# Performance work log

Measured on AMD Instinct MI355X. Metric: run time of the kernel, lower is better.

## Reference

```python
import jax, jax.numpy as jnp
import numpy as np

B, C_IN, C_OUT, N_VERT, K = 8, 64, 64, 40962, 7


def setup_inputs() -> dict:
    key = jax.random.key(0)
    k1, k2, k3, k4 = jax.random.split(key, 4)
    x = jax.random.normal(k1, (B, C_IN, N_VERT), dtype=jnp.float32)
    neigh_indices = jax.random.randint(k2, (N_VERT, K), 0, N_VERT, dtype=jnp.int64)
    # nn.Linear(in=K*C_IN, out=C_OUT): weight [C_OUT, K*C_IN], bias [C_OUT]
    W = jax.random.normal(k3, (C_OUT, C_IN * K), dtype=jnp.float32) * (1.0 / np.sqrt(C_IN * K))
    b = jax.random.normal(k4, (C_OUT,), dtype=jnp.float32) * 0.01
    return {"x": x, "neigh_indices": neigh_indices, "W": W, "b": b}


def reference(x, neigh_indices, W, b):
    # x: [B, C_in, N]; neigh_indices: [N, K]
    # gather neighbor features: [B, C_in, N, K]
    gathered = x[:, :, neigh_indices]
    # Linear over flattened (C_in, K) per vertex. The torch flatten order is
    # (c, k) since mat is [B, N, C_in, K] reshaped to [B*N, C_in*K].
    Wr = W.reshape(W.shape[0], x.shape[1], neigh_indices.shape[1])  # [C_out, C_in, K]
    out = jnp.einsum('bcnk,ock->bon', gathered, Wr) + b[None, :, None]
    return out  # [B, C_out, N]
```

## Files before the change

kernel.cpp:

```cpp
#include <hip/hip_runtime.h>

#define BB 8
#define CI 64
#define CO 64
#define NV 40962
#define KN 7
#define KKD 448

typedef unsigned short u16;
typedef unsigned int u32;

typedef __bf16 bf16x8 __attribute__((ext_vector_type(8)));
typedef float f32x16 __attribute__((ext_vector_type(16)));

__device__ inline u16 f2bf(float f) {
    u32 u = __builtin_bit_cast(u32, f);
    u32 r = (u + 0x7FFFu + ((u >> 16) & 1u)) >> 16;
    return (u16)r;
}

__device__ inline void gload_lds16(const void* g, void* l) {
    __builtin_amdgcn_global_load_lds(
        (const __attribute__((address_space(1))) u32*)g,
        (__attribute__((address_space(3))) u32*)l, 16, 0, 0);
}

__global__ void transpose_x(const float* __restrict__ x, u16* __restrict__ xT) {
    __shared__ u16 tile[64][72];
    const int b = blockIdx.y;
    const int n0 = blockIdx.x * 64;
    const int tid = threadIdx.x;

#pragma unroll
    for (int i = 0; i < 16; ++i) {
        int flat = i * 256 + tid;
        int c = flat >> 6;
        int nn = flat & 63;
        int n = n0 + nn;
        if (n < NV) {
            float v = __builtin_nontemporal_load(&x[((size_t)b * CI + c) * NV + n]);
            tile[nn][c] = f2bf(v);
        }
    }
    __syncthreads();

#pragma unroll
    for (int i = 0; i < 2; ++i) {
        int flat8 = i * 256 + tid;
        int nn = flat8 >> 3;
        int c0 = (flat8 & 7) * 8;
        int n = n0 + nn;
        if (n < NV) {
            uint4 v = *(const uint4*)&tile[nn][c0];
            *(uint4*)&xT[((size_t)b * NV + n) * CI + c0] = v;
        }
    }
}

__global__ void pack_w(const float* __restrict__ W, u16* __restrict__ Wf) {
    int e = blockIdx.x * 256 + threadIdx.x;
    if (e < 2 * 28 * 64 * 8) {
        int j = e & 7;
        int lane = (e >> 3) & 63;
        int sg = e >> 9;
        int s = sg % 28;
        int rg = sg / 28;
        int o = rg * 32 + (lane & 31);
        int kk = s * 16 + ((lane >> 5) << 3) + j;
        int kn = kk >> 6;
        int c = kk & 63;
        Wf[e] = f2bf(W[o * KKD + c * KN + kn]);
    }
}

__global__ __launch_bounds__(512, 4) void conv_mfma(
    const u16* __restrict__ xT, const u16* __restrict__ Wf,
    const int* __restrict__ idx, const float* __restrict__ bias,
    float* __restrict__ out) {
    __shared__ alignas(16) u16 G[3][8192];

    const int bid = blockIdx.x;
    const int b = bid & 7;
    const int n0 = (bid >> 3) * 128;
    const int t = threadIdx.x;
    const int lane = t & 63;
    const int w = t >> 6;
    const int rg = w & 1;
    const int cg = w >> 1;
    const int col = lane & 31;
    const int half = lane >> 5;

    const char* xbc = (const char*)(xT + (size_t)b * NV * CI);
    const char* wfc = (const char*)Wf;

    const int sr0 = t >> 3;
    const int q = t & 7;
    const int qe = q ^ (sr0 & 7);

    int g0 = n0 + sr0;        if (g0 >= NV) g0 = NV - 1;
    int g1 = n0 + 64 + sr0;   if (g1 >= NV) g1 = NV - 1;

    int j0[KN], j1[KN];
    {
        int4 lo0 = *(const int4*)(idx + (size_t)g0 * KN);
        int4 hi0 = *(const int4*)(idx + (size_t)g0 * KN + 3);
        int4 lo1 = *(const int4*)(idx + (size_t)g1 * KN);
        int4 hi1 = *(const int4*)(idx + (size_t)g1 * KN + 3);
        j0[0] = lo0.x; j0[1] = lo0.y; j0[2] = lo0.z; j0[3] = lo0.w;
        j0[4] = hi0.y; j0[5] = hi0.z; j0[6] = hi0.w;
        j1[0] = lo1.x; j1[1] = lo1.y; j1[2] = lo1.z; j1[3] = lo1.w;
        j1[4] = hi1.y; j1[5] = hi1.z; j1[6] = hi1.w;
    }

    char* gb = (char*)&G[0][0];
    const u32 dst0 = (u32)(w * 1024);
    const u32 dst1 = (u32)(8192 + w * 1024);

    const int brow = cg * 32 + col;
    const u32 rbase = (u32)(brow * 128);
    const u32 rmask = (u32)(brow & 7) << 4;

    const u32 abase = (u32)((rg * 28) * 1024 + lane * 16);

    f32x16 acc{};

    gload_lds16(xbc + (size_t)j0[0] * 128 + qe * 16, gb + 0 * 16384 + dst0);
    gload_lds16(xbc + (size_t)j1[0] * 128 + qe * 16, gb + 0 * 16384 + dst1);
    __builtin_amdgcn_sched_barrier(0);
    uint4 acur0 = *(const uint4*)(wfc + abase + 0 * 1024);
    uint4 acur1 = *(const uint4*)(wfc + abase + 1 * 1024);
    uint4 acur2 = *(const uint4*)(wfc + abase + 2 * 1024);
    uint4 acur3 = *(const uint4*)(wfc + abase + 3 * 1024);
    __builtin_amdgcn_sched_barrier(0);
    gload_lds16(xbc + (size_t)j0[1] * 128 + qe * 16, gb + 1 * 16384 + dst0);
    gload_lds16(xbc + (size_t)j1[1] * 128 + qe * 16, gb + 1 * 16384 + dst1);
    __builtin_amdgcn_sched_barrier(0);

#pragma unroll
    for (int k = 0; k < KN; ++k) {
        uint4 an0, an1, an2, an3;
        if (k + 1 < KN) {
            u32 ab = abase + (u32)((k + 1) * 4 * 1024);
            an0 = *(const uint4*)(wfc + ab + 0 * 1024);
            an1 = *(const uint4*)(wfc + ab + 1 * 1024);
            an2 = *(const uint4*)(wfc + ab + 2 * 1024);
            an3 = *(const uint4*)(wfc + ab + 3 * 1024);
        }
        __builtin_amdgcn_sched_barrier(0);

        if (k <= 5) asm volatile("s_waitcnt vmcnt(6)" ::: "memory");
        else        asm volatile("s_waitcnt vmcnt(0)" ::: "memory");
        __builtin_amdgcn_sched_barrier(0);
        __builtin_amdgcn_s_barrier();
        __builtin_amdgcn_sched_barrier(0);

        if (k + 2 < KN) {
            u32 db = (u32)(((k + 2) % 3) * 16384);
            gload_lds16(xbc + (size_t)j0[k + 2] * 128 + qe * 16, gb + db + dst0);
            gload_lds16(xbc + (size_t)j1[k + 2] * 128 + qe * 16, gb + db + dst1);
        }
        __builtin_amdgcn_sched_barrier(0);

        const char* gsrc = gb + (u32)((k % 3) * 16384);
#pragma unroll
        for (int sub = 0; sub < 4; ++sub) {
            u32 boff = rbase + ((((u32)sub * 32) + (u32)half * 16) ^ rmask);
            uint4 bf = *(const uint4*)(gsrc + boff);
            uint4 af = (sub == 0) ? acur0 : (sub == 1) ? acur1 : (sub == 2) ? acur2 : acur3;
            acc = __builtin_amdgcn_mfma_f32_32x32x16_bf16(
                __builtin_bit_cast(bf16x8, af),
                __builtin_bit_cast(bf16x8, bf), acc, 0, 0, 0);
        }

        if (k + 1 < KN) { acur0 = an0; acur1 = an1; acur2 = an2; acur3 = an3; }
    }

    const int v = n0 + cg * 32 + col;
    if (v < NV) {
        float* ob = out + (size_t)b * CO * NV + v;
#pragma unroll
        for (int r = 0; r < 16; ++r) {
            int rowo = (r & 3) + 8 * (r >> 2) + 4 * half;
            int o = rg * 32 + rowo;
            ob[(size_t)o * NV] = acc[r] + bias[o];
        }
    }
}

__global__ void naive_conv(const float* __restrict__ x, const int* __restrict__ idx,
                           const float* __restrict__ W, const float* __restrict__ bias,
                           float* __restrict__ out) {
    const int b = blockIdx.y;
    const int n = blockIdx.x * 4 + (threadIdx.x & 3);
    const int o = threadIdx.x >> 2;
    if (n >= NV) return;
    float acc = bias[o];
    const float* xb = x + (size_t)b * CI * NV;
    const float* wo = W + o * KKD;
    for (int k = 0; k < KN; ++k) {
        int j = idx[n * KN + k];
        for (int c = 0; c < CI; ++c)
            acc += xb[(size_t)c * NV + j] * wo[c * KN + k];
    }
    out[((size_t)b * CO + o) * NV + n] = acc;
}

extern "C" void kernel_launch(void* const* d_in, const int* in_sizes, int n_in,
                              void* d_out, int out_size, void* d_ws, size_t ws_size,
                              hipStream_t stream) {
    const float* x    = (const float*)d_in[0];
    const int*   idx  = (const int*)d_in[1];
    const float* W    = (const float*)d_in[2];
    const float* bias = (const float*)d_in[3];
    float* out = (float*)d_out;

    const size_t xT_bytes = (size_t)BB * NV * CI * 2;
    const size_t wf_bytes = (size_t)2 * 28 * 64 * 8 * 2;
    const size_t need = xT_bytes + wf_bytes;

    if (ws_size >= need) {
        u16* xT = (u16*)d_ws;
        u16* Wf = (u16*)((char*)d_ws + xT_bytes);
        transpose_x<<<dim3((NV + 63) / 64, BB), 256, 0, stream>>>(x, xT);
        pack_w<<<dim3(112), 256, 0, stream>>>(W, Wf);
        const int ntiles = (NV + 127) / 128;
        conv_mfma<<<dim3(ntiles * BB), 512, 0, stream>>>(xT, Wf, idx, bias, out);
    } else {
        naive_conv<<<dim3((NV + 3) / 4, BB), 256, 0, stream>>>(x, idx, W, bias, out);
    }
}
```

Baseline: 80.96 us.

## Interleave batch into vertex-major layout so each gather fetches all batches

The transposed activation buffer changes from [B][N][C] to [N][B][C], so one neighbor index pulls a contiguous 1KB row covering all 8 batches. The conv kernel now tiles 16 vertices times 8 batches per 256-thread block, with each wave running two MFMA accumulators. Index loads and gather requests are shared across batches, which is meant to cut index traffic and improve gather locality. In exchange the grid, swizzle and epilogue are restructured: output stores are scattered across batches and occupancy settings change.

```diff
diff --git a/kernel.cpp b/kernel.cpp
--- a/kernel.cpp
+++ b/kernel.cpp
@@ -25,7 +25,7 @@
         (__attribute__((address_space(3))) u32*)l, 16, 0, 0);
 }
 
-__global__ void transpose_x(const float* __restrict__ x, u16* __restrict__ xT) {
+__global__ void transpose_x(const float* __restrict__ x, u16* __restrict__ xTI) {
     __shared__ u16 tile[64][72];
     const int b = blockIdx.y;
     const int n0 = blockIdx.x * 64;
@@ -52,7 +52,7 @@
         int n = n0 + nn;
         if (n < NV) {
             uint4 v = *(const uint4*)&tile[nn][c0];
-            *(uint4*)&xT[((size_t)b * NV + n) * CI + c0] = v;
+            *(uint4*)&xTI[((size_t)n * 8 + b) * 64 + c0] = v;
         }
     }
 }
@@ -73,67 +73,74 @@
     }
 }
 
-__global__ __launch_bounds__(512, 4) void conv_mfma(
-    const u16* __restrict__ xT, const u16* __restrict__ Wf,
+__global__ __launch_bounds__(256, 3) void conv_mfma(
+    const u16* __restrict__ xTI, const u16* __restrict__ Wf,
     const int* __restrict__ idx, const float* __restrict__ bias,
     float* __restrict__ out) {
     __shared__ alignas(16) u16 G[3][8192];
 
     const int bid = blockIdx.x;
-    const int b = bid & 7;
-    const int n0 = (bid >> 3) * 128;
+    const int n0 = bid * 16;
     const int t = threadIdx.x;
     const int lane = t & 63;
     const int w = t >> 6;
     const int rg = w & 1;
     const int cg = w >> 1;
-    const int col = lane & 31;
     const int half = lane >> 5;
-
-    const char* xbc = (const char*)(xT + (size_t)b * NV * CI);
+    const int seg = lane >> 3;
+    const int sl = lane & 7;
+
+    const char* xbc = (const char*)xTI;
     const char* wfc = (const char*)Wf;
-
-    const int sr0 = t >> 3;
-    const int q = t & 7;
-    const int qe = q ^ (sr0 & 7);
-
-    int g0 = n0 + sr0;        if (g0 >= NV) g0 = NV - 1;
-    int g1 = n0 + 64 + sr0;   if (g1 >= NV) g1 = NV - 1;
-
-    int j0[KN], j1[KN];
-    {
-        int4 lo0 = *(const int4*)(idx + (size_t)g0 * KN);
-        int4 hi0 = *(const int4*)(idx + (size_t)g0 * KN + 3);
-        int4 lo1 = *(const int4*)(idx + (size_t)g1 * KN);
-        int4 hi1 = *(const int4*)(idx + (size_t)g1 * KN + 3);
-        j0[0] = lo0.x; j0[1] = lo0.y; j0[2] = lo0.z; j0[3] = lo0.w;
-        j0[4] = hi0.y; j0[5] = hi0.z; j0[6] = hi0.w;
-        j1[0] = lo1.x; j1[1] = lo1.y; j1[2] = lo1.z; j1[3] = lo1.w;
-        j1[4] = hi1.y; j1[5] = hi1.z; j1[6] = hi1.w;
-    }
-
     char* gb = (char*)&G[0][0];
-    const u32 dst0 = (u32)(w * 1024);
-    const u32 dst1 = (u32)(8192 + w * 1024);
-
-    const int brow = cg * 32 + col;
-    const u32 rbase = (u32)(brow * 128);
-    const u32 rmask = (u32)(brow & 7) << 4;
+
+    int jv[4][KN];
+#pragma unroll
+    for (int i = 0; i < 4; ++i) {
+        int v = n0 + w * 4 + i; if (v >= NV) v = NV - 1;
+        int4 lo = *(const int4*)(idx + (size_t)v * KN);
+        int4 hi = *(const int4*)(idx + (size_t)v * KN + 3);
+        jv[i][0] = lo.x; jv[i][1] = lo.y; jv[i][2] = lo.z; jv[i][3] = lo.w;
+        jv[i][4] = hi.y; jv[i][5] = hi.z; jv[i][6] = hi.w;
+    }
+
+    u32 srcoff[4];
+#pragma unroll
+    for (int i = 0; i < 4; ++i)
+        srcoff[i] = (u32)(seg * 128) + (u32)((((sl ^ seg ^ i) & 7)) << 4);
+
+    const u32 dstrow = (u32)((w * 4) * 1024);
+
+    const int vsub = (lane & 31) >> 3;
+    const int bb = lane & 7;
+    u32 rbyte[2][4];
+#pragma unroll
+    for (int ct = 0; ct < 2; ++ct)
+#pragma unroll
+        for (int s = 0; s < 4; ++s) {
+            int rowv = (cg * 2 + ct) * 4 + vsub;
+            int slot = ((s * 2 + half) ^ bb ^ vsub) & 7;
+            rbyte[ct][s] = (u32)(rowv * 1024 + bb * 128 + slot * 16);
+        }
 
     const u32 abase = (u32)((rg * 28) * 1024 + lane * 16);
 
-    f32x16 acc{};
-
-    gload_lds16(xbc + (size_t)j0[0] * 128 + qe * 16, gb + 0 * 16384 + dst0);
-    gload_lds16(xbc + (size_t)j1[0] * 128 + qe * 16, gb + 0 * 16384 + dst1);
+    f32x16 acc0{}, acc1{};
+
+#pragma unroll
+    for (int i = 0; i < 4; ++i)
+        gload_lds16(xbc + (size_t)jv[i][0] * 1024 + srcoff[i],
+                    gb + 0 * 16384 + dstrow + (u32)(i * 1024));
     __builtin_amdgcn_sched_barrier(0);
     uint4 acur0 = *(const uint4*)(wfc + abase + 0 * 1024);
     uint4 acur1 = *(const uint4*)(wfc + abase + 1 * 1024);
     uint4 acur2 = *(const uint4*)(wfc + abase + 2 * 1024);
     uint4 acur3 = *(const uint4*)(wfc + abase + 3 * 1024);
     __builtin_amdgcn_sched_barrier(0);
-    gload_lds16(xbc + (size_t)j0[1] * 128 + qe * 16, gb + 1 * 16384 + dst0);
-    gload_lds16(xbc + (size_t)j1[1] * 128 + qe * 16, gb + 1 * 16384 + dst1);
+#pragma unroll
+    for (int i = 0; i < 4; ++i)
+        gload_lds16(xbc + (size_t)jv[i][1] * 1024 + srcoff[i],
+                    gb + 1 * 16384 + dstrow + (u32)(i * 1024));
     __builtin_amdgcn_sched_barrier(0);
 
 #pragma unroll
@@ -148,7 +155,7 @@
         }
         __builtin_amdgcn_sched_barrier(0);
 
-        if (k <= 5) asm volatile("s_waitcnt vmcnt(6)" ::: "memory");
+        if (k <= 5) asm volatile("s_waitcnt vmcnt(8)" ::: "memory");
         else        asm volatile("s_waitcnt vmcnt(0)" ::: "memory");
         __builtin_amdgcn_sched_barrier(0);
         __builtin_amdgcn_s_barrier();
@@ -156,34 +163,39 @@
 
         if (k + 2 < KN) {
             u32 db = (u32)(((k + 2) % 3) * 16384);
-            gload_lds16(xbc + (size_t)j0[k + 2] * 128 + qe * 16, gb + db + dst0);
-            gload_lds16(xbc + (size_t)j1[k + 2] * 128 + qe * 16, gb + db + dst1);
+#pragma unroll
+            for (int i = 0; i < 4; ++i)
+                gload_lds16(xbc + (size_t)jv[i][k + 2] * 1024 + srcoff[i],
+                            gb + db + dstrow + (u32)(i * 1024));
         }
         __builtin_amdgcn_sched_barrier(0);
 
         const char* gsrc = gb + (u32)((k % 3) * 16384);
 #pragma unroll
-        for (int sub = 0; sub < 4; ++sub) {
-            u32 boff = rbase + ((((u32)sub * 32) + (u32)half * 16) ^ rmask);
-            uint4 bf = *(const uint4*)(gsrc + boff);
-            uint4 af = (sub == 0) ? acur0 : (sub == 1) ? acur1 : (sub == 2) ? acur2 : acur3;
-            acc = __builtin_amdgcn_mfma_f32_32x32x16_bf16(
-                __builtin_bit_cast(bf16x8, af),
-                __builtin_bit_cast(bf16x8, bf), acc, 0, 0, 0);
+        for (int s = 0; s < 4; ++s) {
+            uint4 b0 = *(const uint4*)(gsrc + rbyte[0][s]);
+            uint4 b1 = *(const uint4*)(gsrc + rbyte[1][s]);
+            uint4 af = (s == 0) ? acur0 : (s == 1) ? acur1 : (s == 2) ? acur2 : acur3;
+            acc0 = __builtin_amdgcn_mfma_f32_32x32x16_bf16(
+                __builtin_bit_cast(bf16x8, af), __builtin_bit_cast(bf16x8, b0), acc0, 0, 0, 0);
+            acc1 = __builtin_amdgcn_mfma_f32_32x32x16_bf16(
+                __builtin_bit_cast(bf16x8, af), __builtin_bit_cast(bf16x8, b1), acc1, 0, 0, 0);
         }
 
         if (k + 1 < KN) { acur0 = an0; acur1 = an1; acur2 = an2; acur3 = an3; }
     }
 
-    const int v = n0 + cg * 32 + col;
-    if (v < NV) {
-        float* ob = out + (size_t)b * CO * NV + v;
-#pragma unroll
-        for (int r = 0; r < 16; ++r) {
-            int rowo = (r & 3) + 8 * (r >> 2) + 4 * half;
-            int o = rg * 32 + rowo;
-            ob[(size_t)o * NV] = acc[r] + bias[o];
-        }
+    const int vb = n0 + cg * 8;
+#pragma unroll
+    for (int r = 0; r < 16; ++r) {
+        int rowo = (r & 3) + 8 * (r >> 2) + 4 * half;
+        int o = rg * 32 + rowo;
+        float bo = bias[o];
+        size_t obase = ((size_t)(bb * CO + o)) * NV;
+        int v0 = vb + vsub;
+        int v1 = vb + 4 + vsub;
+        if (v0 < NV) out[obase + v0] = acc0[r] + bo;
+        if (v1 < NV) out[obase + v1] = acc1[r] + bo;
     }
 }
 
@@ -214,17 +226,17 @@
     const float* bias = (const float*)d_in[3];
     float* out = (float*)d_out;
 
-    const size_t xT_bytes = (size_t)BB * NV * CI * 2;
+    const size_t xT_bytes = (size_t)NV * 8 * CI * 2;
     const size_t wf_bytes = (size_t)2 * 28 * 64 * 8 * 2;
     const size_t need = xT_bytes + wf_bytes;
 
     if (ws_size >= need) {
-        u16* xT = (u16*)d_ws;
+        u16* xTI = (u16*)d_ws;
         u16* Wf = (u16*)((char*)d_ws + xT_bytes);
-        transpose_x<<<dim3((NV + 63) / 64, BB), 256, 0, stream>>>(x, xT);
+        transpose_x<<<dim3((NV + 63) / 64, BB), 256, 0, stream>>>(x, xTI);
         pack_w<<<dim3(112), 256, 0, stream>>>(W, Wf);
-        const int ntiles = (NV + 127) / 128;
-        conv_mfma<<<dim3(ntiles * BB), 512, 0, stream>>>(xT, Wf, idx, bias, out);
+        const int ntiles = (NV + 15) / 16;
+        conv_mfma<<<dim3(ntiles), 256, 0, stream>>>(xTI, Wf, idx, bias, out);
     } else {
         naive_conv<<<dim3((NV + 3) / 4, BB), 256, 0, stream>>>(x, idx, W, bias, out);
     }
```

Measured after the change: 108.3 us. 33.7% more time.
